# Kernel tuning notes

Measured on AMD Instinct MI355X. Metric: run time of the kernel, lower is better.

## Reference

```python
import jax, jax.numpy as jnp
import numpy as np
from jax import lax

B, CIN, COUT = 8, 256, 4
Z = X = Y = 32


def _blur_kernel(c, dtype):
    k = jnp.array([1.0, 1.7, 1.0], dtype=dtype)
    k3 = jnp.einsum('i,j,k->ijk', k, k, k)
    k3 = k3 / k3.sum()  # normalized=True in filter3d
    return jnp.broadcast_to(k3[None, None], (c, 1, 3, 3, 3))


def setup_inputs() -> dict:
    key = jax.random.key(0)
    k1, k2, k3, k4 = jax.random.split(key, 4)
    x = jax.random.normal(k1, (B, CIN, Z, X, Y), dtype=jnp.float32)
    S = jax.random.normal(k2, (B, CIN), dtype=jnp.float32)
    prev = jax.random.normal(k3, (B, COUT, Z, X, Y), dtype=jnp.float32)
    # ModulatedConv3d weight (out, in, 1, 1, 1) -> stored squeezed as (out, in)
    weight = jax.random.normal(k4, (COUT, CIN), dtype=jnp.float32)
    return {"x": x, "S": S, "prev": prev, "weight": weight}


def reference(x, S, prev, weight):
    # Modulated 1x1x1 conv (demodulate=False):
    # out[b,o,z,x,y] = sum_i weight[o,i] * (S[b,i] + 1) * x[b,i,z,x,y]
    xm = x * (S + 1.0)[:, :, None, None, None]
    y = jnp.einsum('oi,bizxy->bozxy', weight, xm)
    y = y + prev
    # Trilinear upsample x2, align_corners=False (half-pixel centers)
    b, c, z, h, w = y.shape
    y = jax.image.resize(y, (b, c, 2 * z, 2 * h, 2 * w), method='trilinear')
    # Blur3d: depthwise 3x3x3 normalized separable kernel, replicate padding
    kern = _blur_kernel(c, y.dtype)
    yp = jnp.pad(y, ((0, 0), (0, 0), (1, 1), (1, 1), (1, 1)), mode='edge')
    out = lax.conv_general_dilated(
        yp, kern, window_strides=(1, 1, 1), padding='VALID',
        dimension_numbers=('NCDHW', 'OIDHW', 'NCDHW'),
        feature_group_count=c)
    return out
```

## Files before the change

### kernel.cpp

```cpp
#include <hip/hip_runtime.h>

#define ZDIM  32
#define SP    (ZDIM * ZDIM * ZDIM)
#define SP4   (SP / 4)
#define CIN   256
#define COUT  4
#define BATCH 8

__device__ __forceinline__ void fma4(float4& a, const float4& v, float w) {
    a.x = fmaf(v.x, w, a.x);
    a.y = fmaf(v.y, w, a.y);
    a.z = fmaf(v.z, w, a.z);
    a.w = fmaf(v.w, w, a.w);
}

__global__ __launch_bounds__(128) void modconv_kernel(
    const float* __restrict__ x, const float* __restrict__ S,
    const float* __restrict__ prev, const float* __restrict__ weight,
    float* __restrict__ y)
{
    __shared__ float wm[CIN * COUT];
    const int b   = blockIdx.y;
    const int tid = threadIdx.x;

    for (int i = tid; i < CIN; i += 128) {
        float s = S[b * CIN + i] + 1.0f;
        #pragma unroll
        for (int o = 0; o < COUT; ++o)
            wm[i * COUT + o] = weight[o * CIN + i] * s;
    }
    __syncthreads();

    const int p4 = blockIdx.x * 128 + tid;
    const float4* xb = (const float4*)x    + (size_t)b * CIN  * SP4 + p4;
    const float4* pv = (const float4*)prev + (size_t)b * COUT * SP4 + p4;
    float4*       yb = (float4*)y          + (size_t)b * COUT * SP4 + p4;

    float4 acc0 = pv[0 * SP4];
    float4 acc1 = pv[1 * SP4];
    float4 acc2 = pv[2 * SP4];
    float4 acc3 = pv[3 * SP4];

    const float4* wm4 = (const float4*)wm;

    #pragma unroll 1
    for (int i = 0; i < CIN; i += 8) {
        float4 xv[8];
        #pragma unroll
        for (int u = 0; u < 8; ++u)
            xv[u] = xb[(size_t)(i + u) * SP4];
        #pragma unroll
        for (int u = 0; u < 8; ++u) {
            float4 w4 = wm4[i + u];
            fma4(acc0, xv[u], w4.x);
            fma4(acc1, xv[u], w4.y);
            fma4(acc2, xv[u], w4.z);
            fma4(acc3, xv[u], w4.w);
        }
    }
    yb[0 * SP4] = acc0;
    yb[1 * SP4] = acc1;
    yb[2 * SP4] = acc2;
    yb[3 * SP4] = acc3;
}

__global__ __launch_bounds__(256) void upblur_kernel(
    const float* __restrict__ y, float* __restrict__ out)
{
    constexpr float wA = 1.175f / 3.7f;
    constexpr float wB = 2.275f / 3.7f;
    constexpr float wC = 0.25f  / 3.7f;

    const int c  = blockIdx.x * 256 + threadIdx.x;
    const int ky = c & 31;
    const int kx = (c >> 5) & 31;
    const int kz = (c >> 10) & 31;
    const int bo = c >> 15;

    const float* yb = y + (size_t)bo * SP;
    const int zs[3] = { max(kz - 1, 0), kz, min(kz + 1, 31) };
    const int xs[3] = { max(kx - 1, 0), kx, min(kx + 1, 31) };
    const int ym = max(ky - 1, 0), yp = min(ky + 1, 31);

    float se[3][3], so[3][3];
    #pragma unroll
    for (int a = 0; a < 3; ++a) {
        #pragma unroll
        for (int b2 = 0; b2 < 3; ++b2) {
            const float* row = yb + zs[a] * (ZDIM * ZDIM) + xs[b2] * ZDIM;
            float v0 = row[ym], v1 = row[ky], v2 = row[yp];
            se[a][b2] = wA * v0 + wB * v1 + wC * v2;
            so[a][b2] = wC * v0 + wB * v1 + wA * v2;
        }
    }
    float t[2][2][3];
    #pragma unroll
    for (int a = 0; a < 3; ++a) {
        t[0][0][a] = wA * se[a][0] + wB * se[a][1] + wC * se[a][2];
        t[1][0][a] = wC * se[a][0] + wB * se[a][1] + wA * se[a][2];
        t[0][1][a] = wA * so[a][0] + wB * so[a][1] + wC * so[a][2];
        t[1][1][a] = wC * so[a][0] + wB * so[a][1] + wA * so[a][2];
    }
    const size_t obase = (size_t)bo * (64 * 64 * 64)
                       + (size_t)(2 * kz) * (64 * 64)
                       + (size_t)(2 * kx) * 64 + 2 * ky;
    #pragma unroll
    for (int pz = 0; pz < 2; ++pz) {
        const float w0 = pz ? wC : wA;
        const float w2 = pz ? wA : wC;
        #pragma unroll
        for (int px = 0; px < 2; ++px) {
            float oy0 = w0 * t[px][0][0] + wB * t[px][0][1] + w2 * t[px][0][2];
            float oy1 = w0 * t[px][1][0] + wB * t[px][1][1] + w2 * t[px][1][2];
            *(float2*)(out + obase + (size_t)pz * (64 * 64) + px * 64) =
                make_float2(oy0, oy1);
        }
    }
}

extern "C" void kernel_launch(void* const* d_in, const int* in_sizes, int n_in,
                              void* d_out, int out_size, void* d_ws, size_t ws_size,
                              hipStream_t stream) {
    const float* x      = (const float*)d_in[0];
    const float* S      = (const float*)d_in[1];
    const float* prev   = (const float*)d_in[2];
    const float* weight = (const float*)d_in[3];
    float* out = (float*)d_out;
    float* y   = (float*)d_ws;

    dim3 g1(SP4 / 128, BATCH);
    modconv_kernel<<<g1, 128, 0, stream>>>(x, S, prev, weight, y);

    const int cells = BATCH * COUT * SP;
    upblur_kernel<<<cells / 256, 256, 0, stream>>>(y, out);
}
```

Baseline: 375.2 us.

## Split channel reduction across two thread halves in modconv kernel

Doubles the modconv block size to 256 threads. Each half reduces 128 of the 256 input channels for the same spatial positions, and the partial sums are combined through shared memory together with the prev residual. This is meant to raise the number of waves and outstanding memory loads in flight. The cost is an extra barrier and a shared-memory partial buffer, and half the threads sit idle during the final write.

```diff
diff --git a/kernel.cpp b/kernel.cpp
--- a/kernel.cpp
+++ b/kernel.cpp
@@ -14,37 +14,36 @@
     a.w = fmaf(v.w, w, a.w);
 }
 
-__global__ __launch_bounds__(128) void modconv_kernel(
+__global__ __launch_bounds__(256) void modconv_kernel(
     const float* __restrict__ x, const float* __restrict__ S,
     const float* __restrict__ prev, const float* __restrict__ weight,
     float* __restrict__ y)
 {
-    __shared__ float wm[CIN * COUT];
-    const int b   = blockIdx.y;
-    const int tid = threadIdx.x;
+    __shared__ float  wm[CIN * COUT];
+    __shared__ float4 part[COUT][128];
 
-    for (int i = tid; i < CIN; i += 128) {
-        float s = S[b * CIN + i] + 1.0f;
+    const int b    = blockIdx.y;
+    const int tid  = threadIdx.x;
+    const int half = tid >> 7;
+    const int t    = tid & 127;
+
+    if (tid < CIN) {
+        float s = S[b * CIN + tid] + 1.0f;
         #pragma unroll
         for (int o = 0; o < COUT; ++o)
-            wm[i * COUT + o] = weight[o * CIN + i] * s;
+            wm[tid * COUT + o] = weight[o * CIN + tid] * s;
     }
     __syncthreads();
 
-    const int p4 = blockIdx.x * 128 + tid;
-    const float4* xb = (const float4*)x    + (size_t)b * CIN  * SP4 + p4;
-    const float4* pv = (const float4*)prev + (size_t)b * COUT * SP4 + p4;
-    float4*       yb = (float4*)y          + (size_t)b * COUT * SP4 + p4;
+    const int p4 = blockIdx.x * 128 + t;
+    const float4* xb = (const float4*)x + (size_t)b * CIN * SP4 + p4;
 
-    float4 acc0 = pv[0 * SP4];
-    float4 acc1 = pv[1 * SP4];
-    float4 acc2 = pv[2 * SP4];
-    float4 acc3 = pv[3 * SP4];
-
+    float4 acc0 = {0,0,0,0}, acc1 = {0,0,0,0}, acc2 = {0,0,0,0}, acc3 = {0,0,0,0};
     const float4* wm4 = (const float4*)wm;
+    const int i0 = half << 7;
 
     #pragma unroll 1
-    for (int i = 0; i < CIN; i += 8) {
+    for (int i = i0; i < i0 + 128; i += 8) {
         float4 xv[8];
         #pragma unroll
         for (int u = 0; u < 8; ++u)
@@ -58,10 +57,31 @@
             fma4(acc3, xv[u], w4.w);
         }
     }
-    yb[0 * SP4] = acc0;
-    yb[1 * SP4] = acc1;
-    yb[2 * SP4] = acc2;
-    yb[3 * SP4] = acc3;
+
+    if (half) {
+        part[0][t] = acc0;
+        part[1][t] = acc1;
+        part[2][t] = acc2;
+        part[3][t] = acc3;
+    }
+    __syncthreads();
+    if (!half) {
+        const float4* pv = (const float4*)prev + (size_t)b * COUT * SP4 + p4;
+        float4*       yb = (float4*)y          + (size_t)b * COUT * SP4 + p4;
+        float4 po, pr;
+        po = part[0][t]; pr = pv[0 * SP4];
+        yb[0 * SP4] = make_float4(acc0.x + po.x + pr.x, acc0.y + po.y + pr.y,
+                                  acc0.z + po.z + pr.z, acc0.w + po.w + pr.w);
+        po = part[1][t]; pr = pv[1 * SP4];
+        yb[1 * SP4] = make_float4(acc1.x + po.x + pr.x, acc1.y + po.y + pr.y,
+                                  acc1.z + po.z + pr.z, acc1.w + po.w + pr.w);
+        po = part[2][t]; pr = pv[2 * SP4];
+        yb[2 * SP4] = make_float4(acc2.x + po.x + pr.x, acc2.y + po.y + pr.y,
+                                  acc2.z + po.z + pr.z, acc2.w + po.w + pr.w);
+        po = part[3][t]; pr = pv[3 * SP4];
+        yb[3 * SP4] = make_float4(acc3.x + po.x + pr.x, acc3.y + po.y + pr.y,
+                                  acc3.z + po.z + pr.z, acc3.w + po.w + pr.w);
+    }
 }
 
 __global__ __launch_bounds__(256) void upblur_kernel(
@@ -129,7 +149,7 @@
     float* y   = (float*)d_ws;
 
     dim3 g1(SP4 / 128, BATCH);
-    modconv_kernel<<<g1, 128, 0, stream>>>(x, S, prev, weight, y);
+    modconv_kernel<<<g1, 256, 0, stream>>>(x, S, prev, weight, y);
 
     const int cells = BATCH * COUT * SP;
     upblur_kernel<<<cells / 256, 256, 0, stream>>>(y, out);
```

Result: slower. 386.9 us (+3.1%).

## Use float2 per thread with nontemporal loads/stores in modconv and upblur

Applied to the files above, without the earlier changes.

The modconv kernel now has each thread handle two spatial elements instead of four, which doubles the grid to get more waves in flight on the streaming read of x. Loads of x and stores of the final output use nontemporal builtins so streaming data does not pollute the cache. The prev tensor is read only at the end and added to the zero-initialized accumulators, which shortens its register lifetime. In exchange, each load request is narrower, so more load instructions are issued per byte.

```diff
diff --git a/kernel.cpp b/kernel.cpp
--- a/kernel.cpp
+++ b/kernel.cpp
@@ -2,16 +2,16 @@
 
 #define ZDIM  32
 #define SP    (ZDIM * ZDIM * ZDIM)
-#define SP4   (SP / 4)
+#define SP2   (SP / 2)
 #define CIN   256
 #define COUT  4
 #define BATCH 8
 
-__device__ __forceinline__ void fma4(float4& a, const float4& v, float w) {
+typedef float vf2 __attribute__((ext_vector_type(2)));
+
+__device__ __forceinline__ void fma2(vf2& a, const vf2& v, float w) {
     a.x = fmaf(v.x, w, a.x);
     a.y = fmaf(v.y, w, a.y);
-    a.z = fmaf(v.z, w, a.z);
-    a.w = fmaf(v.w, w, a.w);
 }
 
 __global__ __launch_bounds__(128) void modconv_kernel(
@@ -31,37 +31,34 @@
     }
     __syncthreads();
 
-    const int p4 = blockIdx.x * 128 + tid;
-    const float4* xb = (const float4*)x    + (size_t)b * CIN  * SP4 + p4;
-    const float4* pv = (const float4*)prev + (size_t)b * COUT * SP4 + p4;
-    float4*       yb = (float4*)y          + (size_t)b * COUT * SP4 + p4;
+    const int p2 = blockIdx.x * 128 + tid;
+    const vf2* xb = (const vf2*)x    + (size_t)b * CIN  * SP2 + p2;
+    const vf2* pv = (const vf2*)prev + (size_t)b * COUT * SP2 + p2;
+    vf2*       yb = (vf2*)y          + (size_t)b * COUT * SP2 + p2;
 
-    float4 acc0 = pv[0 * SP4];
-    float4 acc1 = pv[1 * SP4];
-    float4 acc2 = pv[2 * SP4];
-    float4 acc3 = pv[3 * SP4];
-
+    vf2 acc0 = {0,0}, acc1 = {0,0}, acc2 = {0,0}, acc3 = {0,0};
     const float4* wm4 = (const float4*)wm;
 
     #pragma unroll 1
     for (int i = 0; i < CIN; i += 8) {
-        float4 xv[8];
+        vf2 xv[8];
         #pragma unroll
         for (int u = 0; u < 8; ++u)
-            xv[u] = xb[(size_t)(i + u) * SP4];
+            xv[u] = __builtin_nontemporal_load(&xb[(size_t)(i + u) * SP2]);
         #pragma unroll
         for (int u = 0; u < 8; ++u) {
             float4 w4 = wm4[i + u];
-            fma4(acc0, xv[u], w4.x);
-            fma4(acc1, xv[u], w4.y);
-            fma4(acc2, xv[u], w4.z);
-            fma4(acc3, xv[u], w4.w);
+            fma2(acc0, xv[u], w4.x);
+            fma2(acc1, xv[u], w4.y);
+            fma2(acc2, xv[u], w4.z);
+            fma2(acc3, xv[u], w4.w);
         }
     }
-    yb[0 * SP4] = acc0;
-    yb[1 * SP4] = acc1;
-    yb[2 * SP4] = acc2;
-    yb[3 * SP4] = acc3;
+    vf2 pr;
+    pr = pv[0 * SP2]; yb[0 * SP2] = acc0 + pr;
+    pr = pv[1 * SP2]; yb[1 * SP2] = acc1 + pr;
+    pr = pv[2 * SP2]; yb[2 * SP2] = acc2 + pr;
+    pr = pv[3 * SP2]; yb[3 * SP2] = acc3 + pr;
 }
 
 __global__ __launch_bounds__(256) void upblur_kernel(
@@ -112,8 +109,9 @@
         for (int px = 0; px < 2; ++px) {
             float oy0 = w0 * t[px][0][0] + wB * t[px][0][1] + w2 * t[px][0][2];
             float oy1 = w0 * t[px][1][0] + wB * t[px][1][1] + w2 * t[px][1][2];
-            *(float2*)(out + obase + (size_t)pz * (64 * 64) + px * 64) =
-                make_float2(oy0, oy1);
+            vf2 v = {oy0, oy1};
+            __builtin_nontemporal_store(
+                v, (vf2*)(out + obase + (size_t)pz * (64 * 64) + px * 64));
         }
     }
 }
@@ -128,7 +126,7 @@
     float* out = (float*)d_out;
     float* y   = (float*)d_ws;
 
-    dim3 g1(SP4 / 128, BATCH);
+    dim3 g1(SP2 / 128, BATCH);
     modconv_kernel<<<g1, 128, 0, stream>>>(x, S, prev, weight, y);
 
     const int cells = BATCH * COUT * SP;
```

Measured after the change: 359.9 us. 1.04x faster.
